# Performance work log

Measured on AMD Instinct MI355X. Metric: run time of the kernel, lower is better.

## Reference

```python
import jax, jax.numpy as jnp
import numpy as np

HEADS = 20  # head_dim = 1280 // 20 = 64
LORA_SCALE = 1.0


def setup_inputs() -> dict:
    key = jax.random.key(0)
    ks = jax.random.split(key, 16)
    B, S, C, R = 2, 2048, 1280, 4
    w = 0.02  # keep activations numerically tame
    inp = {
        "x": jax.random.normal(ks[0], (B, S, C), jnp.float32),
        "Wq": jax.random.normal(ks[1], (C, C), jnp.float32) * w,
        "Wk": jax.random.normal(ks[2], (C, C), jnp.float32) * w,
        "Wv": jax.random.normal(ks[3], (C, C), jnp.float32) * w,
        "Wo": jax.random.normal(ks[4], (C, C), jnp.float32) * w,
        "bo": jnp.zeros((C,), jnp.float32),
        "Aq": jax.random.normal(ks[5], (R, C), jnp.float32) * w,
        "Bq": jax.random.normal(ks[6], (C, R), jnp.float32) * w,
        "Ak": jax.random.normal(ks[7], (R, C), jnp.float32) * w,
        "Bk": jax.random.normal(ks[8], (C, R), jnp.float32) * w,
        "Av": jax.random.normal(ks[9], (R, C), jnp.float32) * w,
        "Bv": jax.random.normal(ks[10], (C, R), jnp.float32) * w,
        "Ao": jax.random.normal(ks[11], (R, C), jnp.float32) * w,
        "Bo": jax.random.normal(ks[12], (C, R), jnp.float32) * w,
    }
    return inp


def _lora(x, A, B):
    # LoRALinearLayer: up(down(x)); network_alpha=None -> no extra scaling
    return (x @ A.T) @ B.T


def reference(x, Wq, Wk, Wv, Wo, bo, Aq, Bq, Ak, Bk, Av, Bv, Ao, Bo):
    B, S, C = x.shape
    H = HEADS
    D = C // H
    # base projections + LoRA updates (self-attention: encoder_hidden_states = x)
    q = x @ Wq.T + LORA_SCALE * _lora(x, Aq, Bq)
    k = x @ Wk.T + LORA_SCALE * _lora(x, Ak, Bk)
    v = x @ Wv.T + LORA_SCALE * _lora(x, Av, Bv)
    # head split: [B, S, H, D]
    q = q.reshape(B, S, H, D)
    k = k.reshape(B, S, H, D)
    v = v.reshape(B, S, H, D)
    # explicit scores + softmax (attn.get_attention_scores), scale = 1/sqrt(D)
    scale = 1.0 / jnp.sqrt(jnp.asarray(D, x.dtype))
    scores = jnp.einsum("bshd,bthd->bhst", q, k) * scale  # [B, H, S, S]
    probs = jax.nn.softmax(scores, axis=-1)
    ctx = jnp.einsum("bhst,bthd->bshd", probs, v).reshape(B, S, C)
    # output projection (+bias) + LoRA; dropout is identity at eval
    out = ctx @ Wo.T + bo + LORA_SCALE * _lora(ctx, Ao, Bo)
    return out
```

## Files before the change

### kernel.cpp

```cpp
#include <hip/hip_runtime.h>

#define BATCH 2
#define SEQ   2048
#define CH    1280
#define NH    20
#define HD    64
#define BS    (BATCH*SEQ)
#define RK    4

typedef __attribute__((ext_vector_type(4)))  short bf16x4;
typedef __attribute__((ext_vector_type(8)))  short bf16x8;
typedef __attribute__((ext_vector_type(4)))  float floatx4;
typedef __attribute__((ext_vector_type(16))) float floatx16;

__device__ __forceinline__ floatx4 mfma16(bf16x8 a, bf16x8 b, floatx4 c) {
    return __builtin_amdgcn_mfma_f32_16x16x32_bf16(a, b, c, 0, 0, 0);
}
__device__ __forceinline__ floatx16 mfma32(bf16x8 a, bf16x8 b, floatx16 c) {
    return __builtin_amdgcn_mfma_f32_32x32x16_bf16(a, b, c, 0, 0, 0);
}
__device__ __forceinline__ floatx16 mfma32k8(bf16x4 a, bf16x4 b, floatx16 c) {
    return __builtin_amdgcn_mfma_f32_32x32x8bf16_1k(a, b, c, 0, 0, 0);
}

__device__ __forceinline__ unsigned short f2bf(float f) {
    unsigned int u = __float_as_uint(f);
    u += 0x7fffu + ((u >> 16) & 1u);
    return (unsigned short)(u >> 16);
}
__device__ __forceinline__ unsigned int packbf(float hi, float lo) {
    unsigned int a = __float_as_uint(hi) + 0x8000u;
    unsigned int b = __float_as_uint(lo) + 0x8000u;
    return __builtin_amdgcn_perm(a, b, 0x07060302u);
}
__device__ __forceinline__ float fexp2(float x) {
#if __has_builtin(__builtin_amdgcn_exp2f)
    return __builtin_amdgcn_exp2f(x);
#else
    return exp2f(x);
#endif
}

__device__ __forceinline__ void cp16(const unsigned short* g, unsigned short* l) {
    __builtin_amdgcn_global_load_lds(
        (const __attribute__((address_space(1))) unsigned int*)g,
        (__attribute__((address_space(3))) unsigned int*)l, 16, 0, 0);
}

__global__ __launch_bounds__(256) void fold_weights(
    const float* __restrict__ Wq, const float* __restrict__ Wk,
    const float* __restrict__ Wv, const float* __restrict__ Wo,
    const float* __restrict__ Aq, const float* __restrict__ Bq,
    const float* __restrict__ Ak, const float* __restrict__ Bk,
    const float* __restrict__ Av, const float* __restrict__ Bv,
    const float* __restrict__ Ao, const float* __restrict__ Bo,
    unsigned short* __restrict__ wq_bf, unsigned short* __restrict__ wk_bf,
    unsigned short* __restrict__ wv_bf, unsigned short* __restrict__ wo_bf)
{
    int e = blockIdx.x * 256 + threadIdx.x;
    int which = blockIdx.y;
    int i = e / CH, j = e % CH;
    const float *W, *A, *Bm;
    unsigned short* o;
    if (which == 0)      { W = Wq; A = Aq; Bm = Bq; o = wq_bf; }
    else if (which == 1) { W = Wk; A = Ak; Bm = Bk; o = wk_bf; }
    else if (which == 2) { W = Wv; A = Av; Bm = Bv; o = wv_bf; }
    else                 { W = Wo; A = Ao; Bm = Bo; o = wo_bf; }
    float acc = W[e];
#pragma unroll
    for (int r = 0; r < RK; r++) acc += Bm[i * RK + r] * A[r * CH + j];
    o[e] = f2bf(acc);
}

__global__ __launch_bounds__(256) void cast_x(const float* __restrict__ x,
                                              unsigned short* __restrict__ xb)
{
    int idx = (blockIdx.x * 256 + threadIdx.x) * 4;
    float4 v = *(const float4*)(x + idx);
    ushort4 o;
    o.x = f2bf(v.x); o.y = f2bf(v.y); o.z = f2bf(v.z); o.w = f2bf(v.w);
    *(ushort4*)(xb + idx) = o;
}

template<bool OUTF>
__device__ __forceinline__ void gemm128(
    const unsigned short* __restrict__ A, const unsigned short* __restrict__ B,
    unsigned short* __restrict__ obf, float* __restrict__ of,
    const float* __restrict__ bias, float oscale)
{
    __shared__ __align__(16) unsigned short sa[128 * 32];
    __shared__ __align__(16) unsigned short sb[128 * 32];
    const int tid = threadIdx.x;
    const int wav = tid >> 6, lane = tid & 63, m16 = lane & 15, quad = lane >> 4;
    const int wr = wav >> 1, wc = wav & 1;
    const int M0 = blockIdx.y * 128, N0 = blockIdx.x * 128;

    const int s0 = tid, s1 = tid + 256;
    const int row0 = s0 >> 2, row1 = s1 >> 2;
    const int cc0 = (s0 & 3) ^ ((row0 + (row0 >> 2)) & 3);
    const int cc1 = (s1 & 3) ^ ((row1 + (row1 >> 2)) & 3);
    const unsigned short* ga0 = A + (size_t)(M0 + row0) * CH + cc0 * 8;
    const unsigned short* ga1 = A + (size_t)(M0 + row1) * CH + cc1 * 8;
    const unsigned short* gb0 = B + (size_t)(N0 + row0) * CH + cc0 * 8;
    const unsigned short* gb1 = B + (size_t)(N0 + row1) * CH + cc1 * 8;
    unsigned short* la0 = sa + (size_t)(wav * 64) * 8;
    unsigned short* la1 = sa + (size_t)(wav * 64 + 256) * 8;
    unsigned short* lb0 = sb + (size_t)(wav * 64) * 8;
    unsigned short* lb1 = sb + (size_t)(wav * 64 + 256) * 8;

    const unsigned short* af[4]; const unsigned short* bfp[4];
#pragma unroll
    for (int mt = 0; mt < 4; mt++) {
        int row = wr * 64 + mt * 16 + m16;
        af[mt] = sa + row * 32 + ((quad ^ ((row + (row >> 2)) & 3)) << 3);
    }
#pragma unroll
    for (int nt = 0; nt < 4; nt++) {
        int row = wc * 64 + nt * 16 + m16;
        bfp[nt] = sb + row * 32 + ((quad ^ ((row + (row >> 2)) & 3)) << 3);
    }

    floatx4 acc[4][4];
#pragma unroll
    for (int a = 0; a < 4; a++)
#pragma unroll
        for (int b = 0; b < 4; b++) acc[a][b] = (floatx4){0.f, 0.f, 0.f, 0.f};

    for (int k0 = 0; k0 < CH; k0 += 32) {
        cp16(ga0, la0); cp16(ga1, la1); cp16(gb0, lb0); cp16(gb1, lb1);
        ga0 += 32; ga1 += 32; gb0 += 32; gb1 += 32;
        __syncthreads();
        bf16x8 a[4], b[4];
#pragma unroll
        for (int mt = 0; mt < 4; mt++) a[mt] = *(const bf16x8*)af[mt];
#pragma unroll
        for (int nt = 0; nt < 4; nt++) b[nt] = *(const bf16x8*)bfp[nt];
#pragma unroll
        for (int mt = 0; mt < 4; mt++)
#pragma unroll
            for (int nt = 0; nt < 4; nt++)
                acc[mt][nt] = mfma16(a[mt], b[nt], acc[mt][nt]);
        __syncthreads();
    }

#pragma unroll
    for (int mt = 0; mt < 4; mt++) {
#pragma unroll
        for (int nt = 0; nt < 4; nt++) {
            int col = N0 + wc * 64 + nt * 16 + m16;
            float bv = OUTF ? bias[col] : 0.f;
#pragma unroll
            for (int r = 0; r < 4; r++) {
                size_t row = (size_t)(M0 + wr * 64 + mt * 16 + quad * 4 + r);
                if (OUTF) of[row * CH + col] = acc[mt][nt][r] + bv;
                else      obf[row * CH + col] = f2bf(acc[mt][nt][r] * oscale);
            }
        }
    }
}

__global__ __launch_bounds__(256) void gemm_qkv(
    const unsigned short* __restrict__ xb,
    const unsigned short* __restrict__ wq, const unsigned short* __restrict__ wk,
    const unsigned short* __restrict__ wv,
    unsigned short* __restrict__ q, unsigned short* __restrict__ k,
    unsigned short* __restrict__ v)
{
    const unsigned short* w = blockIdx.z == 0 ? wq : blockIdx.z == 1 ? wk : wv;
    unsigned short* o = blockIdx.z == 0 ? q : blockIdx.z == 1 ? k : v;
    float scale = blockIdx.z == 0 ? 0.18033688011112042f : 1.0f;
    gemm128<false>(xb, w, o, nullptr, nullptr, scale);
}

__global__ __launch_bounds__(256) void gemm_o(
    const unsigned short* __restrict__ c_bf, const unsigned short* __restrict__ wo,
    const float* __restrict__ bias, float* __restrict__ out)
{
    gemm128<true>(c_bf, wo, nullptr, out, bias, 1.0f);
}

__global__ __launch_bounds__(256) void transpose_v(
    const unsigned short* __restrict__ v, unsigned short* __restrict__ vt)
{
    __shared__ unsigned short lds[32][34];
    const int s0 = blockIdx.x * 32;
    const int d0 = blockIdx.y * 32;
    const int bh = blockIdx.z, b = bh / NH, h = bh % NH;
    const int c = threadIdx.x & 31;
    const int rbase = threadIdx.x >> 5;
#pragma unroll
    for (int i = 0; i < 4; i++) {
        int r = rbase + i * 8;
        lds[r][c] = v[(size_t)(b * SEQ + s0 + r) * CH + h * HD + d0 + c];
    }
    __syncthreads();
#pragma unroll
    for (int i = 0; i < 4; i++) {
        int r = rbase + i * 8;
        vt[(size_t)(bh * HD + d0 + r) * SEQ + s0 + c] = lds[c][r];
    }
}

__global__ __launch_bounds__(256) void attention(
    const unsigned short* __restrict__ q, const unsigned short* __restrict__ k,
    const unsigned short* __restrict__ vt, unsigned short* __restrict__ c_bf)
{
    __shared__ __align__(16) unsigned short k_lds[128 * 64];
    __shared__ __align__(16) unsigned short v_lds[64 * 128];

    const int tid = threadIdx.x, wav = tid >> 6, lane = tid & 63;
    const int n32 = lane & 31, half = lane >> 5;
    const int q0 = blockIdx.x * 128;
    const int bh = blockIdx.y, b = bh / NH, h = bh % NH;

    const size_t qrow = (size_t)(b * SEQ + q0 + wav * 32 + n32);
    bf16x8 qf[4];
#pragma unroll
    for (int f = 0; f < 4; f++)
        qf[f] = *(const bf16x8*)(q + qrow * CH + h * HD + f * 16 + half * 8);

    const unsigned short* gk[4]; const unsigned short* gv[4];
    unsigned short* lk[4]; unsigned short* lv[4];
#pragma unroll
    for (int g = 0; g < 4; g++) {
        int s = g * 256 + tid;
        int rowk = s >> 3, cck = (s & 7) ^ (rowk & 7);
        gk[g] = k + (size_t)(b * SEQ + rowk) * CH + h * HD + cck * 8;
        lk[g] = k_lds + (size_t)(g * 256 + wav * 64) * 8;
        int rowv = s >> 4, ccv = (s & 15) ^ (rowv & 15);
        gv[g] = vt + (size_t)(bh * HD + rowv) * SEQ + ccv * 8;
        lv[g] = v_lds + (size_t)(g * 256 + wav * 64) * 8;
    }

    float psum = 0.f;
    floatx16 acc[2];
#pragma unroll
    for (int dt = 0; dt < 2; dt++)
#pragma unroll
        for (int r = 0; r < 16; r++) acc[dt][r] = 0.f;

    for (int t0 = 0; t0 < SEQ; t0 += 128) {
#pragma unroll
        for (int g = 0; g < 4; g++) { cp16(gk[g], lk[g]); cp16(gv[g], lv[g]); }
#pragma unroll
        for (int g = 0; g < 4; g++) { gk[g] += (size_t)128 * CH; gv[g] += 128; }
        __syncthreads();

#pragma unroll
        for (int kt = 0; kt < 4; kt++) {
            const int keyrow = kt * 32 + n32;
            const unsigned short* kr = k_lds + keyrow * 64;
            floatx16 st;
#pragma unroll
            for (int r = 0; r < 16; r++) st[r] = 0.f;
#pragma unroll
            for (int f = 0; f < 4; f++) {
                int phys = (2 * f + half) ^ (keyrow & 7);
                bf16x8 kf = *(const bf16x8*)(kr + phys * 8);
                st = mfma32(kf, qf[f], st);
            }

            float p[16];
#pragma unroll
            for (int r = 0; r < 16; r++) { p[r] = fexp2(st[r]); psum += p[r]; }
            unsigned int pk[8];
#pragma unroll
            for (int j = 0; j < 8; j++) pk[j] = packbf(p[2 * j + 1], p[2 * j]);

#pragma unroll
            for (int dt = 0; dt < 2; dt++) {
                const int drow = dt * 32 + n32;
                const unsigned short* vr = v_lds + drow * 128;
#pragma unroll
                for (int g2 = 0; g2 < 4; g2++) {
                    int phys = (kt * 4 + g2) ^ (drow & 15);
                    bf16x4 vf = *(const bf16x4*)(vr + phys * 8 + half * 4);
                    union { unsigned int u[2]; bf16x4 v; } pb;
                    pb.u[0] = pk[2 * g2]; pb.u[1] = pk[2 * g2 + 1];
                    acc[dt] = mfma32k8(vf, pb.v, acc[dt]);
                }
            }
        }
        __syncthreads();
    }

    float tot = psum + __shfl_xor(psum, 32, 64);
    float rinv = __frcp_rn(tot);
    const size_t obase = qrow * CH + h * HD;
#pragma unroll
    for (int dt = 0; dt < 2; dt++) {
#pragma unroll
        for (int jj = 0; jj < 4; jj++) {
            int d = dt * 32 + 8 * jj + 4 * half;
            uint2 o2;
            o2.x = packbf(acc[dt][4 * jj + 1] * rinv, acc[dt][4 * jj + 0] * rinv);
            o2.y = packbf(acc[dt][4 * jj + 3] * rinv, acc[dt][4 * jj + 2] * rinv);
            *(uint2*)(c_bf + obase + d) = o2;
        }
    }
}

extern "C" void kernel_launch(void* const* d_in, const int* in_sizes, int n_in,
                              void* d_out, int out_size, void* d_ws, size_t ws_size,
                              hipStream_t stream)
{
    const float* x  = (const float*)d_in[0];
    const float* Wq = (const float*)d_in[1];
    const float* Wk = (const float*)d_in[2];
    const float* Wv = (const float*)d_in[3];
    const float* Wo = (const float*)d_in[4];
    const float* bo = (const float*)d_in[5];
    const float* Aq = (const float*)d_in[6];
    const float* Bq = (const float*)d_in[7];
    const float* Ak = (const float*)d_in[8];
    const float* Bk = (const float*)d_in[9];
    const float* Av = (const float*)d_in[10];
    const float* Bv = (const float*)d_in[11];
    const float* Ao = (const float*)d_in[12];
    const float* Bo = (const float*)d_in[13];
    float* out = (float*)d_out;

    char* ws = (char*)d_ws;
    size_t off = 0;
    auto alloc = [&](size_t bytes) -> void* {
        void* p = ws + off; off += (bytes + 255) & ~(size_t)255; return p;
    };
    const size_t WB = (size_t)CH * CH, XB = (size_t)BS * CH;
    unsigned short* wq_bf = (unsigned short*)alloc(WB * 2);
    unsigned short* wk_bf = (unsigned short*)alloc(WB * 2);
    unsigned short* wv_bf = (unsigned short*)alloc(WB * 2);
    unsigned short* wo_bf = (unsigned short*)alloc(WB * 2);
    unsigned short* x_bf  = (unsigned short*)alloc(XB * 2);
    unsigned short* q_bf  = (unsigned short*)alloc(XB * 2);
    unsigned short* k_bf  = (unsigned short*)alloc(XB * 2);
    unsigned short* v_bf  = (unsigned short*)alloc(XB * 2);
    unsigned short* vt_bf = (unsigned short*)alloc(XB * 2);
    unsigned short* c_bf  = (unsigned short*)alloc(XB * 2);
    (void)ws_size; (void)n_in; (void)in_sizes; (void)out_size;

    fold_weights<<<dim3(CH * CH / 256, 4), 256, 0, stream>>>(
        Wq, Wk, Wv, Wo, Aq, Bq, Ak, Bk, Av, Bv, Ao, Bo,
        wq_bf, wk_bf, wv_bf, wo_bf);

    cast_x<<<dim3(BS * CH / 1024), 256, 0, stream>>>(x, x_bf);

    gemm_qkv<<<dim3(CH / 128, BS / 128, 3), 256, 0, stream>>>(
        x_bf, wq_bf, wk_bf, wv_bf, q_bf, k_bf, v_bf);

    transpose_v<<<dim3(SEQ / 32, 2, BATCH * NH), 256, 0, stream>>>(v_bf, vt_bf);

    attention<<<dim3(SEQ / 128, BATCH * NH), 256, 0, stream>>>(
        q_bf, k_bf, vt_bf, c_bf);

    gemm_o<<<dim3(CH / 128, BS / 128), 256, 0, stream>>>(c_bf, wo_bf, bo, out);
}
```

Measured before the change: 284.2 us.

## Switch GEMM to 32x32x16 MFMA with K-tile of 64

The 128x128 GEMM tile now uses 32x32x16 bf16 MFMA instructions (2x2 per wave) instead of 16x16x32 (4x4 per wave), and the shared-memory K slice doubles from 32 to 64 with a new XOR swizzle. Each loop iteration does twice the work per barrier pair, which halves synchronisation count and reduces LDS read traffic per MFMA. In exchange, shared memory per block doubles to 32 KB, which may lower occupancy, and the output store pattern changes to the 32x32 accumulator layout.

Result: faster. 277.4 us (-2.4%).

```diff
diff --git a/kernel.cpp b/kernel.cpp
--- a/kernel.cpp
+++ b/kernel.cpp
@@ -10,12 +10,8 @@
 
 typedef __attribute__((ext_vector_type(4)))  short bf16x4;
 typedef __attribute__((ext_vector_type(8)))  short bf16x8;
-typedef __attribute__((ext_vector_type(4)))  float floatx4;
 typedef __attribute__((ext_vector_type(16))) float floatx16;
 
-__device__ __forceinline__ floatx4 mfma16(bf16x8 a, bf16x8 b, floatx4 c) {
-    return __builtin_amdgcn_mfma_f32_16x16x32_bf16(a, b, c, 0, 0, 0);
-}
 __device__ __forceinline__ floatx16 mfma32(bf16x8 a, bf16x8 b, floatx16 c) {
     return __builtin_amdgcn_mfma_f32_32x32x16_bf16(a, b, c, 0, 0, 0);
 }
@@ -88,71 +84,75 @@
     unsigned short* __restrict__ obf, float* __restrict__ of,
     const float* __restrict__ bias, float oscale)
 {
-    __shared__ __align__(16) unsigned short sa[128 * 32];
-    __shared__ __align__(16) unsigned short sb[128 * 32];
+    __shared__ __align__(16) unsigned short sa[128 * 64];
+    __shared__ __align__(16) unsigned short sb[128 * 64];
     const int tid = threadIdx.x;
-    const int wav = tid >> 6, lane = tid & 63, m16 = lane & 15, quad = lane >> 4;
+    const int wav = tid >> 6, lane = tid & 63;
+    const int n32 = lane & 31, half = lane >> 5;
     const int wr = wav >> 1, wc = wav & 1;
     const int M0 = blockIdx.y * 128, N0 = blockIdx.x * 128;
 
-    const int s0 = tid, s1 = tid + 256;
-    const int row0 = s0 >> 2, row1 = s1 >> 2;
-    const int cc0 = (s0 & 3) ^ ((row0 + (row0 >> 2)) & 3);
-    const int cc1 = (s1 & 3) ^ ((row1 + (row1 >> 2)) & 3);
-    const unsigned short* ga0 = A + (size_t)(M0 + row0) * CH + cc0 * 8;
-    const unsigned short* ga1 = A + (size_t)(M0 + row1) * CH + cc1 * 8;
-    const unsigned short* gb0 = B + (size_t)(N0 + row0) * CH + cc0 * 8;
-    const unsigned short* gb1 = B + (size_t)(N0 + row1) * CH + cc1 * 8;
-    unsigned short* la0 = sa + (size_t)(wav * 64) * 8;
-    unsigned short* la1 = sa + (size_t)(wav * 64 + 256) * 8;
-    unsigned short* lb0 = sb + (size_t)(wav * 64) * 8;
-    unsigned short* lb1 = sb + (size_t)(wav * 64 + 256) * 8;
-
-    const unsigned short* af[4]; const unsigned short* bfp[4];
-#pragma unroll
-    for (int mt = 0; mt < 4; mt++) {
-        int row = wr * 64 + mt * 16 + m16;
-        af[mt] = sa + row * 32 + ((quad ^ ((row + (row >> 2)) & 3)) << 3);
-    }
-#pragma unroll
-    for (int nt = 0; nt < 4; nt++) {
-        int row = wc * 64 + nt * 16 + m16;
-        bfp[nt] = sb + row * 32 + ((quad ^ ((row + (row >> 2)) & 3)) << 3);
-    }
-
-    floatx4 acc[4][4];
-#pragma unroll
-    for (int a = 0; a < 4; a++)
-#pragma unroll
-        for (int b = 0; b < 4; b++) acc[a][b] = (floatx4){0.f, 0.f, 0.f, 0.f};
-
-    for (int k0 = 0; k0 < CH; k0 += 32) {
-        cp16(ga0, la0); cp16(ga1, la1); cp16(gb0, lb0); cp16(gb1, lb1);
-        ga0 += 32; ga1 += 32; gb0 += 32; gb1 += 32;
+    const unsigned short* ga[4]; const unsigned short* gb[4];
+    unsigned short* la[4]; unsigned short* lb[4];
+#pragma unroll
+    for (int g = 0; g < 4; g++) {
+        int s = g * 256 + tid;
+        int row = s >> 3, cc = (s & 7) ^ (row & 7);
+        ga[g] = A + (size_t)(M0 + row) * CH + cc * 8;
+        gb[g] = B + (size_t)(N0 + row) * CH + cc * 8;
+        la[g] = sa + (size_t)(g * 256 + wav * 64) * 8;
+        lb[g] = sb + (size_t)(g * 256 + wav * 64) * 8;
+    }
+
+    const int arow0 = wr * 64 + n32, brow0 = wc * 64 + n32;
+
+    floatx16 acc[2][2];
+#pragma unroll
+    for (int mt = 0; mt < 2; mt++)
+#pragma unroll
+        for (int nt = 0; nt < 2; nt++)
+#pragma unroll
+            for (int r = 0; r < 16; r++) acc[mt][nt][r] = 0.f;
+
+    for (int k0 = 0; k0 < CH; k0 += 64) {
+#pragma unroll
+        for (int g = 0; g < 4; g++) { cp16(ga[g], la[g]); cp16(gb[g], lb[g]); }
+#pragma unroll
+        for (int g = 0; g < 4; g++) { ga[g] += 64; gb[g] += 64; }
         __syncthreads();
-        bf16x8 a[4], b[4];
-#pragma unroll
-        for (int mt = 0; mt < 4; mt++) a[mt] = *(const bf16x8*)af[mt];
-#pragma unroll
-        for (int nt = 0; nt < 4; nt++) b[nt] = *(const bf16x8*)bfp[nt];
-#pragma unroll
-        for (int mt = 0; mt < 4; mt++)
-#pragma unroll
-            for (int nt = 0; nt < 4; nt++)
-                acc[mt][nt] = mfma16(a[mt], b[nt], acc[mt][nt]);
+
+        bf16x8 av[2][4], bv[2][4];
+#pragma unroll
+        for (int mt = 0; mt < 2; mt++) {
+            const int ar = arow0 + mt * 32, br = brow0 + mt * 32;
+#pragma unroll
+            for (int ks = 0; ks < 4; ks++) {
+                const int cc = ks * 2 + half;
+                av[mt][ks] = *(const bf16x8*)(sa + ar * 64 + ((cc ^ (ar & 7)) << 3));
+                bv[mt][ks] = *(const bf16x8*)(sb + br * 64 + ((cc ^ (br & 7)) << 3));
+            }
+        }
+#pragma unroll
+        for (int ks = 0; ks < 4; ks++)
+#pragma unroll
+            for (int mt = 0; mt < 2; mt++)
+#pragma unroll
+                for (int nt = 0; nt < 2; nt++)
+                    acc[mt][nt] = mfma32(av[mt][ks], bv[nt][ks], acc[mt][nt]);
         __syncthreads();
     }
 
 #pragma unroll
-    for (int mt = 0; mt < 4; mt++) {
-#pragma unroll
-        for (int nt = 0; nt < 4; nt++) {
-            int col = N0 + wc * 64 + nt * 16 + m16;
-            float bv = OUTF ? bias[col] : 0.f;
-#pragma unroll
-            for (int r = 0; r < 4; r++) {
-                size_t row = (size_t)(M0 + wr * 64 + mt * 16 + quad * 4 + r);
-                if (OUTF) of[row * CH + col] = acc[mt][nt][r] + bv;
+    for (int mt = 0; mt < 2; mt++) {
+#pragma unroll
+        for (int nt = 0; nt < 2; nt++) {
+            const int col = N0 + wc * 64 + nt * 32 + n32;
+            const float bv2 = OUTF ? bias[col] : 0.f;
+#pragma unroll
+            for (int r = 0; r < 16; r++) {
+                size_t row = (size_t)(M0 + wr * 64 + mt * 32 +
+                                      (r & 3) + 8 * (r >> 2) + 4 * half);
+                if (OUTF) of[row * CH + col] = acc[mt][nt][r] + bv2;
                 else      obf[row * CH + col] = f2bf(acc[mt][nt][r] * oscale);
             }
         }
```
